# Kernel tuning notes

Hardware: AMD Instinct MI355X
Metric: run time of the kernel (lower is better)

## Reference

```python
import jax, jax.numpy as jnp
import numpy as np

B, C, L = 4, 512, 2048
H, D = 8, C // 8  # n_heads, attention_size


def conv1d_same(x, w, b):
    # x: [B, C, L], w: [Cout, Cin, 3], b: [Cout]; padding='same'
    y = jax.lax.conv_general_dilated(x, w, window_strides=(1,), padding='SAME',
                                     dimension_numbers=('NCH', 'OIH', 'NCH'))
    return y + b[None, :, None]


def setup_inputs() -> dict:
    key = jax.random.key(0)
    ks = jax.random.split(key, 11)
    s = 0.02
    inp = {
        'q': jax.random.normal(ks[0], (B, C, L), jnp.float32),
        'k': jax.random.normal(ks[1], (B, C, L), jnp.float32),
        'v': jax.random.normal(ks[2], (B, C, L), jnp.float32),
        'wq_w': jax.random.normal(ks[3], (C, C, 3), jnp.float32) * s,
        'wq_b': jnp.zeros((C,), jnp.float32),
        'wk_w': jax.random.normal(ks[4], (C, C, 3), jnp.float32) * s,
        'wk_b': jnp.zeros((C,), jnp.float32),
        'wv_w': jax.random.normal(ks[5], (C, C, 3), jnp.float32) * s,
        'wv_b': jnp.zeros((C,), jnp.float32),
        'fc_w': jax.random.normal(ks[6], (C, C, 3), jnp.float32) * s,
        'fc_b': jnp.zeros((C,), jnp.float32),
    }
    return inp


def reference(q, k, v, wq_w, wq_b, wk_w, wk_b, wv_w, wv_b, fc_w, fc_b):
    b = q.shape[0]
    # Faithful to torch: conv output [B,C,L] is row-major reshaped to [B,L,H,D]
    qh = conv1d_same(q, wq_w, wq_b).reshape(b, -1, H, D).transpose(0, 2, 1, 3)  # [B,H,L,D]
    kh = conv1d_same(k, wk_w, wk_b).reshape(b, -1, H, D).transpose(0, 2, 3, 1)  # [B,H,D,L]
    vh = conv1d_same(v, wv_w, wv_b).reshape(b, -1, H, D).transpose(0, 2, 1, 3)  # [B,H,L,D]
    # NOTE: original divides by attention_size D, not sqrt(D)
    attn = jax.nn.softmax(jnp.matmul(qh, kh) / D, axis=-1)  # [B,H,L,L]
    out = jnp.matmul(attn, vh)                               # [B,H,L,D]
    out = out.transpose(0, 2, 1, 3).reshape(b, H * D, -1)    # [B,C,L]
    return conv1d_same(out, fc_w, fc_b)
```

## Files before the change

### kernel.cpp

```cpp
#include <hip/hip_runtime.h>
#include <hip/hip_bf16.h>

#define BB 4
#define NH 8
#define HD 64
#define CC 512
#define LL 2048
#define KK 1536
#define LPAD 2050

typedef float f32x4 __attribute__((ext_vector_type(4)));
typedef short bf16x8 __attribute__((ext_vector_type(8)));

static __device__ __forceinline__ ushort f2bf(float f) {
  union { float f; unsigned u; } v; v.f = f;
  unsigned r = v.u + 0x7fffu + ((v.u >> 16) & 1u);
  return (ushort)(r >> 16);
}
static __device__ __forceinline__ void gload16(const ushort* g, ushort* l) {
  __builtin_amdgcn_global_load_lds((const __attribute__((address_space(1))) void*)g,
                                   (__attribute__((address_space(3))) void*)l, 16, 0, 0);
}

__global__ void prep_w(const float* __restrict__ w0, const float* __restrict__ w1,
                       const float* __restrict__ w2, const float* __restrict__ w3,
                       ushort* __restrict__ out)
{
  int i = blockIdx.x * 256 + threadIdx.x;
  const int per = CC * KK;
  if (i >= 4 * per) return;
  int cidx = i / per;
  int rem  = i - cidx * per;
  int co   = rem / KK;
  int kk   = rem - co * KK;
  int t = kk >> 9, ci = kk & 511;
  const float* w = (cidx == 0) ? w0 : (cidx == 1) ? w1 : (cidx == 2) ? w2 : w3;
  out[i] = f2bf(w[((size_t)co * CC + ci) * 3 + t]);
}

__device__ __forceinline__ void transpose_body(const float* __restrict__ xb,
                                               ushort* __restrict__ ob)
{
  const int c0 = blockIdx.y * 64;
  const int l0 = blockIdx.x * 64;
  const int tid = threadIdx.x;
  __shared__ ushort T[64 * 72];
  {
    const int rr = tid >> 4;
    const int f4 = tid & 15;
#pragma unroll
    for (int it = 0; it < 4; ++it) {
      const int cc = rr + it * 16;
      ushort s[4];
      float4 vv = *(const float4*)(xb + (size_t)(c0 + cc) * LL + l0 + f4 * 4);
      s[0] = f2bf(vv.x); s[1] = f2bf(vv.y); s[2] = f2bf(vv.z); s[3] = f2bf(vv.w);
      *(ushort4*)&T[cc * 72 + f4 * 4] = *(ushort4*)s;
    }
  }
  __syncthreads();
  {
    const int lr = tid >> 3;
    const int ch = tid & 7;
#pragma unroll
    for (int it = 0; it < 2; ++it) {
      const int ll = lr + it * 32;
      ushort tmp[8];
#pragma unroll
      for (int e = 0; e < 8; ++e) tmp[e] = T[(ch * 8 + e) * 72 + ll];
      *(uint4*)(ob + (size_t)(l0 + ll + 1) * CC + c0 + ch * 8) = *(uint4*)tmp;
    }
  }
  if (blockIdx.x == 0 && tid < 8) {
    uint4 z4 = make_uint4(0, 0, 0, 0);
    *(uint4*)(ob + c0 + tid * 8) = z4;
  }
  if (blockIdx.x == (LL / 64 - 1) && tid >= 248) {
    uint4 z4 = make_uint4(0, 0, 0, 0);
    *(uint4*)(ob + (size_t)(LPAD - 1) * CC + c0 + (tid - 248) * 8) = z4;
  }
}

__global__ __launch_bounds__(256, 4)
void transpose_k(const float* __restrict__ in, ushort* __restrict__ outT)
{
  const int b = blockIdx.z;
  transpose_body(in + (size_t)b * CC * LL, outT + (size_t)b * (LPAD * CC));
}

__global__ __launch_bounds__(256, 4)
void transpose3_k(const float* __restrict__ q, const float* __restrict__ k,
                  const float* __restrict__ v, ushort* __restrict__ xq,
                  ushort* __restrict__ xk, ushort* __restrict__ xv)
{
  const int z = blockIdx.z;
  const int b = z & 3, var = z >> 2;
  const float* in = (var == 0) ? q : (var == 1) ? k : v;
  ushort* out = (var == 0) ? xq : (var == 1) ? xk : xv;
  transpose_body(in + (size_t)b * CC * LL, out + (size_t)b * (LPAD * CC));
}

template<int BM>
__device__ __forceinline__ void conv_body(const ushort* __restrict__ xb,
                                          const ushort* __restrict__ Wt,
                                          const float* __restrict__ bias,
                                          void* __restrict__ outp, int mode, int b)
{
  const int co0 = blockIdx.y * BM;
  const int l0  = blockIdx.x * 128;
  const int tid = threadIdx.x;
  const int lane = tid & 63;
  const int w    = tid >> 6;
  const int col  = lane & 15, quad = lane >> 4;
  constexpr int MI = BM / 32;

  __shared__ ushort Asl[BM * 64];
  __shared__ ushort Bsl[128 * 64];

  const int sr = tid >> 3;
  const int g8 = ((tid & 7) ^ (sr & 7)) * 8;
  const ushort* ag  = Wt + (size_t)(co0 + sr) * KK + g8;
  const ushort* bg  = xb + (size_t)(l0 + sr) * CC + g8;
  ushort* alds = &Asl[tid * 8];
  ushort* blds = &Bsl[tid * 8];

  f32x4 acc[MI][4] = {};
  const int wm = (w & 1) * (BM / 2);
  const int wn = (w >> 1) * 64;
  const int c7 = col & 7;

  for (int k0 = 0; k0 < KK; k0 += 64) {
#pragma unroll
    for (int r2 = 0; r2 < MI; ++r2)
      gload16(ag + (size_t)(r2 * 32) * KK + k0, alds + r2 * 2048);
#pragma unroll
    for (int r2 = 0; r2 < 4; ++r2)
      gload16(bg + (size_t)(r2 * 32) * CC + k0, blds + r2 * 2048);
    __syncthreads();
#pragma unroll
    for (int kk = 0; kk < 2; ++kk) {
      bf16x8 af[MI], bfr[4];
#pragma unroll
      for (int i = 0; i < MI; ++i)
        af[i] = *(const bf16x8*)&Asl[(wm + i * 16 + col) * 64 + (((kk * 4 + quad) ^ c7) * 8)];
#pragma unroll
      for (int j = 0; j < 4; ++j)
        bfr[j] = *(const bf16x8*)&Bsl[(wn + j * 16 + col) * 64 + (((kk * 4 + quad) ^ c7) * 8)];
#pragma unroll
      for (int i = 0; i < MI; ++i)
#pragma unroll
        for (int j = 0; j < 4; ++j)
          acc[i][j] = __builtin_amdgcn_mfma_f32_16x16x32_bf16(af[i], bfr[j], acc[i][j], 0, 0, 0);
    }
    __syncthreads();
  }

#pragma unroll
  for (int i = 0; i < MI; ++i) {
#pragma unroll
    for (int r = 0; r < 4; ++r) {
      const int co = co0 + wm + i * 16 + quad * 4 + r;
      const float bi = bias[co];
#pragma unroll
      for (int j = 0; j < 4; ++j) {
        const int l = l0 + wn + j * 16 + col;
        const float y = acc[i][j][r] + bi;
        if (mode == 0) {
          const int xx = (co << 2) + (l >> 9);
          const int hh = (l >> 6) & 7;
          const int dd = l & 63;
          ((ushort*)outp)[((size_t)(b * NH + hh) * LL + xx) * HD + dd] = f2bf(y);
        } else if (mode == 1) {
          const int xx = (co << 2) + (l >> 9);
          const int hh = (l >> 6) & 7;
          const int dd = l & 63;
          ((ushort*)outp)[((size_t)(b * NH + hh) * HD + dd) * LL + xx] = f2bf(y);
        } else {
          ((float*)outp)[(size_t)(b * CC + co) * LL + l] = y;
        }
      }
    }
  }
}

template<int BM>
__global__ __launch_bounds__(256, 3)
void conv_k(const ushort* __restrict__ xT, const ushort* __restrict__ Wt,
            const float* __restrict__ bias, void* __restrict__ outp, int mode)
{
  const int b = blockIdx.z;
  conv_body<BM>(xT + (size_t)b * (LPAD * CC), Wt, bias, outp, mode, b);
}

__global__ __launch_bounds__(256, 3)
void conv3_k(const ushort* __restrict__ xq, const ushort* __restrict__ xk,
             const ushort* __restrict__ xv, const ushort* __restrict__ Wt,
             const float* __restrict__ b0, const float* __restrict__ b1,
             const float* __restrict__ b2, ushort* __restrict__ o0,
             ushort* __restrict__ o1, ushort* __restrict__ o2)
{
  const int z = blockIdx.z;
  const int b = z & 3, var = z >> 2;
  const ushort* xT = (var == 0) ? xq : (var == 1) ? xk : xv;
  const float* bias = (var == 0) ? b0 : (var == 1) ? b1 : b2;
  ushort* outp = (var == 0) ? o0 : (var == 1) ? o1 : o2;
  conv_body<128>(xT + (size_t)b * (LPAD * CC), Wt + (size_t)var * CC * KK, bias, outp,
                 (var == 2) ? 1 : 0, b);
}

__global__ __launch_bounds__(256, 2)
void attn_k(const ushort* __restrict__ qh, const ushort* __restrict__ kh,
            const ushort* __restrict__ vt, ushort* __restrict__ obT)
{
  const int id   = blockIdx.x;
  const int xcd  = id & 7;
  const int slot = id >> 3;
  const int bh   = xcd * 4 + (slot >> 4);
  const int x0   = (slot & 15) * 128;
  const int b = bh >> 3, h = bh & 7;
  const int tid = threadIdx.x, lane = tid & 63, wv = tid >> 6;
  const int col = lane & 15, quad = lane >> 4;
  const int wx = wv * 32;
  const int c7 = col & 7;

  __shared__ ushort Kv[2][8192];
  __shared__ ushort Ps[128 * 88];

  const ushort* Qg = qh + (size_t)bh * (LL * HD);
  const ushort* Kg = kh + (size_t)bh * (LL * HD);
  const ushort* Vg = vt + (size_t)bh * (HD * LL);
  ushort* ob = obT + (size_t)b * (LPAD * CC);

  const int sr = tid >> 3;
  const int g8 = ((tid & 7) ^ (sr & 7)) * 8;

  bf16x8 aq[2][2];
#pragma unroll
  for (int i = 0; i < 2; ++i)
#pragma unroll
    for (int kk = 0; kk < 2; ++kk)
      aq[i][kk] = *(const bf16x8*)(Qg + (size_t)(x0 + wx + i * 16 + col) * HD + kk * 32 + quad * 8);

  const short one = (short)0x3F80;
  const bf16x8 ones = {one, one, one, one, one, one, one, one};

  f32x4 oacc[2][4] = {};
  f32x4 dacc[2] = {};

  {
    ushort* kb = &Kv[0][tid * 8];
    gload16(Kg + (size_t)sr * HD + g8, kb);
    gload16(Kg + (size_t)(32 + sr) * HD + g8, kb + 2048);
    gload16(Vg + (size_t)sr * LL + g8, kb + 4096);
    gload16(Vg + (size_t)(32 + sr) * LL + g8, kb + 6144);
  }

  for (int yt = 0; yt < 32; ++yt) {
    const int cur = yt & 1;
    __syncthreads();
    if (yt + 1 < 32) {
      const int y1 = (yt + 1) * 64;
      ushort* kb = &Kv[1 - cur][tid * 8];
      gload16(Kg + (size_t)(y1 + sr) * HD + g8, kb);
      gload16(Kg + (size_t)(y1 + 32 + sr) * HD + g8, kb + 2048);
      gload16(Vg + (size_t)sr * LL + y1 + g8, kb + 4096);
      gload16(Vg + (size_t)(32 + sr) * LL + y1 + g8, kb + 6144);
    }
    const ushort* Kb = &Kv[cur][0];
    const ushort* Vb = &Kv[cur][4096];

    f32x4 sacc[4][2] = {};
#pragma unroll
    for (int kk = 0; kk < 2; ++kk)
#pragma unroll
      for (int j = 0; j < 4; ++j) {
        bf16x8 bk = *(const bf16x8*)&Kb[(j * 16 + col) * 64 + (((kk * 4 + quad) ^ c7) * 8)];
        sacc[j][0] = __builtin_amdgcn_mfma_f32_16x16x32_bf16(bk, aq[0][kk], sacc[j][0], 0, 0, 0);
        sacc[j][1] = __builtin_amdgcn_mfma_f32_16x16x32_bf16(bk, aq[1][kk], sacc[j][1], 0, 0, 0);
      }
#pragma unroll
    for (int j = 0; j < 4; ++j)
#pragma unroll
      for (int i = 0; i < 2; ++i) {
        union { __hip_bfloat162 h[2]; uint2 u; } pk;
        pk.h[0] = __float22bfloat162_rn(make_float2(__expf(sacc[j][i][0] * 0.015625f),
                                                   __expf(sacc[j][i][1] * 0.015625f)));
        pk.h[1] = __float22bfloat162_rn(make_float2(__expf(sacc[j][i][2] * 0.015625f),
                                                   __expf(sacc[j][i][3] * 0.015625f)));
        *(uint2*)&Ps[(wx + i * 16 + col) * 88 + j * 16 + quad * 4] = pk.u;
      }
#pragma unroll
    for (int kk = 0; kk < 2; ++kk) {
      bf16x8 ap0 = *(const bf16x8*)&Ps[(wx + col) * 88 + kk * 32 + quad * 8];
      bf16x8 ap1 = *(const bf16x8*)&Ps[(wx + 16 + col) * 88 + kk * 32 + quad * 8];
      dacc[0] = __builtin_amdgcn_mfma_f32_16x16x32_bf16(ap0, ones, dacc[0], 0, 0, 0);
      dacc[1] = __builtin_amdgcn_mfma_f32_16x16x32_bf16(ap1, ones, dacc[1], 0, 0, 0);
#pragma unroll
      for (int j = 0; j < 4; ++j) {
        bf16x8 bv = *(const bf16x8*)&Vb[(j * 16 + col) * 64 + (((kk * 4 + quad) ^ c7) * 8)];
        oacc[0][j] = __builtin_amdgcn_mfma_f32_16x16x32_bf16(ap0, bv, oacc[0][j], 0, 0, 0);
        oacc[1][j] = __builtin_amdgcn_mfma_f32_16x16x32_bf16(ap1, bv, oacc[1][j], 0, 0, 0);
      }
    }
  }

#pragma unroll
  for (int i = 0; i < 2; ++i) {
#pragma unroll
    for (int r = 0; r < 4; ++r) {
      const int xg = x0 + wx + i * 16 + quad * 4 + r;
      const float inv = 1.f / dacc[i][r];
#pragma unroll
      for (int j = 0; j < 4; ++j) {
        const int d = j * 16 + col;
        const int flat = xg * 512 + h * 64 + d;
        const int c = flat >> 11, l = flat & 2047;
        ob[(size_t)(l + 1) * CC + c] = f2bf(oacc[i][j][r] * inv);
      }
    }
  }
  if ((slot & 15) == 0 && tid < 128) {
    const int rw = tid >> 6;
    const int cc = h * 64 + (tid & 63);
    ob[(size_t)(rw ? (LPAD - 1) : 0) * CC + cc] = 0;
  }
}

extern "C" void kernel_launch(void* const* d_in, const int* in_sizes, int n_in,
                              void* d_out, int out_size, void* d_ws, size_t ws_size,
                              hipStream_t stream) {
  const float* q    = (const float*)d_in[0];
  const float* k    = (const float*)d_in[1];
  const float* v    = (const float*)d_in[2];
  const float* wq_w = (const float*)d_in[3];
  const float* wq_b = (const float*)d_in[4];
  const float* wk_w = (const float*)d_in[5];
  const float* wk_b = (const float*)d_in[6];
  const float* wv_w = (const float*)d_in[7];
  const float* wv_b = (const float*)d_in[8];
  const float* fc_w = (const float*)d_in[9];
  const float* fc_b = (const float*)d_in[10];

  char* ws = (char*)d_ws;
  const size_t WSZ = (size_t)CC * KK * sizeof(ushort);
  const size_t HSZ = (size_t)BB * NH * LL * HD * sizeof(ushort);
  const size_t XSZ = (size_t)BB * LPAD * CC * sizeof(ushort);
  const size_t FUSED_NEED = 4 * WSZ + 3 * HSZ + 3 * XSZ;

  ushort* Wt = (ushort*)(ws);
  prep_w<<<(4 * CC * KK + 255) / 256, 256, 0, stream>>>(wq_w, wk_w, wv_w, fc_w, Wt);

  if (ws_size >= FUSED_NEED) {
    ushort* qh  = (ushort*)(ws + 4 * WSZ);
    ushort* kh  = (ushort*)(ws + 4 * WSZ + HSZ);
    ushort* vt  = (ushort*)(ws + 4 * WSZ + 2 * HSZ);
    ushort* xTq = (ushort*)(ws + 4 * WSZ + 3 * HSZ);
    ushort* xTk = (ushort*)(ws + 4 * WSZ + 3 * HSZ + XSZ);
    ushort* xTv = (ushort*)(ws + 4 * WSZ + 3 * HSZ + 2 * XSZ);
    ushort* obT = xTq;

    transpose3_k<<<dim3(32, 8, 12), 256, 0, stream>>>(q, k, v, xTq, xTk, xTv);
    conv3_k<<<dim3(16, 4, 12), 256, 0, stream>>>(xTq, xTk, xTv, Wt,
                                                 wq_b, wk_b, wv_b, qh, kh, vt);
    attn_k<<<512, 256, 0, stream>>>(qh, kh, vt, obT);
    conv_k<64><<<dim3(16, 8, 4), 256, 0, stream>>>(obT, Wt + 3 * CC * KK, fc_b,
                                                   (float*)d_out, 2);
  } else {
    ushort* qh  = (ushort*)(ws + 4 * WSZ);
    ushort* kh  = (ushort*)(ws + 4 * WSZ + HSZ);
    ushort* vt  = (ushort*)(ws + 4 * WSZ + 2 * HSZ);
    ushort* xTb = (ushort*)(ws + 4 * WSZ + 3 * HSZ);
    ushort* obT = xTb;

    transpose_k<<<dim3(32, 8, 4), 256, 0, stream>>>(q, xTb);
    conv_k<128><<<dim3(16, 4, 4), 256, 0, stream>>>(xTb, Wt + 0 * CC * KK, wq_b, qh, 0);
    transpose_k<<<dim3(32, 8, 4), 256, 0, stream>>>(k, xTb);
    conv_k<128><<<dim3(16, 4, 4), 256, 0, stream>>>(xTb, Wt + 1 * CC * KK, wk_b, kh, 0);
    transpose_k<<<dim3(32, 8, 4), 256, 0, stream>>>(v, xTb);
    conv_k<128><<<dim3(16, 4, 4), 256, 0, stream>>>(xTb, Wt + 2 * CC * KK, wv_b, vt, 1);
    attn_k<<<512, 256, 0, stream>>>(qh, kh, vt, obT);
    conv_k<64><<<dim3(16, 8, 4), 256, 0, stream>>>(obT, Wt + 3 * CC * KK, fc_b,
                                                   (float*)d_out, 2);
  }
}
```

Baseline: 257.3 us.

## Fold softmax scale into Q conv epilogue and double attention block threads

The Q projection epilogue now multiplies by log2(e)/D, so the attention kernel can use raw exp2 instead of a scaled expf. The attention kernel moves to 512 threads per block with each wave owning 16 query rows instead of 32. The per-wave accumulators and Q fragments shrink, which is meant to raise occupancy and give more waves to hide latency. Each thread now issues half as many K/V tile loads. In exchange there are more waves per block to synchronize, and each wave reuses each K/V fragment for fewer MFMAs, raising LDS read traffic per MFMA.

```diff
diff --git a/kernel.cpp b/kernel.cpp
--- a/kernel.cpp
+++ b/kernel.cpp
@@ -8,6 +8,8 @@
 #define LL 2048
 #define KK 1536
 #define LPAD 2050
+
+#define QS 0.022542110013890054f
 
 typedef float f32x4 __attribute__((ext_vector_type(4)));
 typedef short bf16x8 __attribute__((ext_vector_type(8)));
@@ -103,7 +105,8 @@
 __device__ __forceinline__ void conv_body(const ushort* __restrict__ xb,
                                           const ushort* __restrict__ Wt,
                                           const float* __restrict__ bias,
-                                          void* __restrict__ outp, int mode, int b)
+                                          void* __restrict__ outp, int mode, int b,
+                                          float scale)
 {
   const int co0 = blockIdx.y * BM;
   const int l0  = blockIdx.x * 128;
@@ -163,7 +166,7 @@
 #pragma unroll
       for (int j = 0; j < 4; ++j) {
         const int l = l0 + wn + j * 16 + col;
-        const float y = acc[i][j][r] + bi;
+        const float y = (acc[i][j][r] + bi) * scale;
         if (mode == 0) {
           const int xx = (co << 2) + (l >> 9);
           const int hh = (l >> 6) & 7;
@@ -185,10 +188,11 @@
 template<int BM>
 __global__ __launch_bounds__(256, 3)
 void conv_k(const ushort* __restrict__ xT, const ushort* __restrict__ Wt,
-            const float* __restrict__ bias, void* __restrict__ outp, int mode)
+            const float* __restrict__ bias, void* __restrict__ outp, int mode,
+            float scale)
 {
   const int b = blockIdx.z;
-  conv_body<BM>(xT + (size_t)b * (LPAD * CC), Wt, bias, outp, mode, b);
+  conv_body<BM>(xT + (size_t)b * (LPAD * CC), Wt, bias, outp, mode, b, scale);
 }
 
 __global__ __launch_bounds__(256, 3)
@@ -203,11 +207,12 @@
   const ushort* xT = (var == 0) ? xq : (var == 1) ? xk : xv;
   const float* bias = (var == 0) ? b0 : (var == 1) ? b1 : b2;
   ushort* outp = (var == 0) ? o0 : (var == 1) ? o1 : o2;
+  const float scale = (var == 0) ? QS : 1.0f;
   conv_body<128>(xT + (size_t)b * (LPAD * CC), Wt + (size_t)var * CC * KK, bias, outp,
-                 (var == 2) ? 1 : 0, b);
-}
-
-__global__ __launch_bounds__(256, 2)
+                 (var == 2) ? 1 : 0, b, scale);
+}
+
+__global__ __launch_bounds__(512, 4)
 void attn_k(const ushort* __restrict__ qh, const ushort* __restrict__ kh,
             const ushort* __restrict__ vt, ushort* __restrict__ obT)
 {
@@ -219,7 +224,7 @@
   const int b = bh >> 3, h = bh & 7;
   const int tid = threadIdx.x, lane = tid & 63, wv = tid >> 6;
   const int col = lane & 15, quad = lane >> 4;
-  const int wx = wv * 32;
+  const int wx = wv * 16;
   const int c7 = col & 7;
 
   __shared__ ushort Kv[2][8192];
@@ -233,25 +238,20 @@
   const int sr = tid >> 3;
   const int g8 = ((tid & 7) ^ (sr & 7)) * 8;
 
-  bf16x8 aq[2][2];
-#pragma unroll
-  for (int i = 0; i < 2; ++i)
-#pragma unroll
-    for (int kk = 0; kk < 2; ++kk)
-      aq[i][kk] = *(const bf16x8*)(Qg + (size_t)(x0 + wx + i * 16 + col) * HD + kk * 32 + quad * 8);
+  bf16x8 aq[2];
+#pragma unroll
+  for (int kk = 0; kk < 2; ++kk)
+    aq[kk] = *(const bf16x8*)(Qg + (size_t)(x0 + wx + col) * HD + kk * 32 + quad * 8);
 
   const short one = (short)0x3F80;
   const bf16x8 ones = {one, one, one, one, one, one, one, one};
 
-  f32x4 oacc[2][4] = {};
-  f32x4 dacc[2] = {};
+  f32x4 oacc[4] = {};
+  f32x4 dacc = {};
 
   {
-    ushort* kb = &Kv[0][tid * 8];
-    gload16(Kg + (size_t)sr * HD + g8, kb);
-    gload16(Kg + (size_t)(32 + sr) * HD + g8, kb + 2048);
-    gload16(Vg + (size_t)sr * LL + g8, kb + 4096);
-    gload16(Vg + (size_t)(32 + sr) * LL + g8, kb + 6144);
+    gload16(Kg + (size_t)sr * HD + g8, &Kv[0][tid * 8]);
+    gload16(Vg + (size_t)sr * LL + g8, &Kv[0][4096 + tid * 8]);
   }
 
   for (int yt = 0; yt < 32; ++yt) {
@@ -259,63 +259,51 @@
     __syncthreads();
     if (yt + 1 < 32) {
       const int y1 = (yt + 1) * 64;
-      ushort* kb = &Kv[1 - cur][tid * 8];
-      gload16(Kg + (size_t)(y1 + sr) * HD + g8, kb);
-      gload16(Kg + (size_t)(y1 + 32 + sr) * HD + g8, kb + 2048);
-      gload16(Vg + (size_t)sr * LL + y1 + g8, kb + 4096);
-      gload16(Vg + (size_t)(32 + sr) * LL + y1 + g8, kb + 6144);
+      gload16(Kg + (size_t)(y1 + sr) * HD + g8, &Kv[1 - cur][tid * 8]);
+      gload16(Vg + (size_t)sr * LL + y1 + g8, &Kv[1 - cur][4096 + tid * 8]);
     }
     const ushort* Kb = &Kv[cur][0];
     const ushort* Vb = &Kv[cur][4096];
 
-    f32x4 sacc[4][2] = {};
+    f32x4 sacc[4] = {};
 #pragma unroll
     for (int kk = 0; kk < 2; ++kk)
 #pragma unroll
       for (int j = 0; j < 4; ++j) {
         bf16x8 bk = *(const bf16x8*)&Kb[(j * 16 + col) * 64 + (((kk * 4 + quad) ^ c7) * 8)];
-        sacc[j][0] = __builtin_amdgcn_mfma_f32_16x16x32_bf16(bk, aq[0][kk], sacc[j][0], 0, 0, 0);
-        sacc[j][1] = __builtin_amdgcn_mfma_f32_16x16x32_bf16(bk, aq[1][kk], sacc[j][1], 0, 0, 0);
+        sacc[j] = __builtin_amdgcn_mfma_f32_16x16x32_bf16(bk, aq[kk], sacc[j], 0, 0, 0);
       }
 #pragma unroll
-    for (int j = 0; j < 4; ++j)
-#pragma unroll
-      for (int i = 0; i < 2; ++i) {
-        union { __hip_bfloat162 h[2]; uint2 u; } pk;
-        pk.h[0] = __float22bfloat162_rn(make_float2(__expf(sacc[j][i][0] * 0.015625f),
-                                                   __expf(sacc[j][i][1] * 0.015625f)));
-        pk.h[1] = __float22bfloat162_rn(make_float2(__expf(sacc[j][i][2] * 0.015625f),
-                                                   __expf(sacc[j][i][3] * 0.015625f)));
-        *(uint2*)&Ps[(wx + i * 16 + col) * 88 + j * 16 + quad * 4] = pk.u;
-      }
+    for (int j = 0; j < 4; ++j) {
+      union { __hip_bfloat162 h[2]; uint2 u; } pk;
+      pk.h[0] = __float22bfloat162_rn(make_float2(__builtin_amdgcn_exp2f(sacc[j][0]),
+                                                 __builtin_amdgcn_exp2f(sacc[j][1])));
+      pk.h[1] = __float22bfloat162_rn(make_float2(__builtin_amdgcn_exp2f(sacc[j][2]),
+                                                 __builtin_amdgcn_exp2f(sacc[j][3])));
+      *(uint2*)&Ps[(wx + col) * 88 + j * 16 + quad * 4] = pk.u;
+    }
 #pragma unroll
     for (int kk = 0; kk < 2; ++kk) {
-      bf16x8 ap0 = *(const bf16x8*)&Ps[(wx + col) * 88 + kk * 32 + quad * 8];
-      bf16x8 ap1 = *(const bf16x8*)&Ps[(wx + 16 + col) * 88 + kk * 32 + quad * 8];
-      dacc[0] = __builtin_amdgcn_mfma_f32_16x16x32_bf16(ap0, ones, dacc[0], 0, 0, 0);
-      dacc[1] = __builtin_amdgcn_mfma_f32_16x16x32_bf16(ap1, ones, dacc[1], 0, 0, 0);
+      bf16x8 ap = *(const bf16x8*)&Ps[(wx + col) * 88 + kk * 32 + quad * 8];
+      dacc = __builtin_amdgcn_mfma_f32_16x16x32_bf16(ap, ones, dacc, 0, 0, 0);
 #pragma unroll
       for (int j = 0; j < 4; ++j) {
         bf16x8 bv = *(const bf16x8*)&Vb[(j * 16 + col) * 64 + (((kk * 4 + quad) ^ c7) * 8)];
-        oacc[0][j] = __builtin_amdgcn_mfma_f32_16x16x32_bf16(ap0, bv, oacc[0][j], 0, 0, 0);
-        oacc[1][j] = __builtin_amdgcn_mfma_f32_16x16x32_bf16(ap1, bv, oacc[1][j], 0, 0, 0);
+        oacc[j] = __builtin_amdgcn_mfma_f32_16x16x32_bf16(ap, bv, oacc[j], 0, 0, 0);
       }
     }
   }
 
 #pragma unroll
-  for (int i = 0; i < 2; ++i) {
-#pragma unroll
-    for (int r = 0; r < 4; ++r) {
-      const int xg = x0 + wx + i * 16 + quad * 4 + r;
-      const float inv = 1.f / dacc[i][r];
-#pragma unroll
-      for (int j = 0; j < 4; ++j) {
-        const int d = j * 16 + col;
-        const int flat = xg * 512 + h * 64 + d;
-        const int c = flat >> 11, l = flat & 2047;
-        ob[(size_t)(l + 1) * CC + c] = f2bf(oacc[i][j][r] * inv);
-      }
+  for (int r = 0; r < 4; ++r) {
+    const int xg = x0 + wx + quad * 4 + r;
+    const float inv = 1.f / dacc[r];
+#pragma unroll
+    for (int j = 0; j < 4; ++j) {
+      const int d = j * 16 + col;
+      const int flat = xg * 512 + h * 64 + d;
+      const int c = flat >> 11, l = flat & 2047;
+      ob[(size_t)(l + 1) * CC + c] = f2bf(oacc[j][r] * inv);
     }
   }
   if ((slot & 15) == 0 && tid < 128) {
@@ -361,9 +349,9 @@
     transpose3_k<<<dim3(32, 8, 12), 256, 0, stream>>>(q, k, v, xTq, xTk, xTv);
     conv3_k<<<dim3(16, 4, 12), 256, 0, stream>>>(xTq, xTk, xTv, Wt,
                                                  wq_b, wk_b, wv_b, qh, kh, vt);
-    attn_k<<<512, 256, 0, stream>>>(qh, kh, vt, obT);
+    attn_k<<<512, 512, 0, stream>>>(qh, kh, vt, obT);
     conv_k<64><<<dim3(16, 8, 4), 256, 0, stream>>>(obT, Wt + 3 * CC * KK, fc_b,
-                                                   (float*)d_out, 2);
+                                                   (float*)d_out, 2, 1.0f);
   } else {
     ushort* qh  = (ushort*)(ws + 4 * WSZ);
     ushort* kh  = (ushort*)(ws + 4 * WSZ + HSZ);
@@ -372,13 +360,13 @@
     ushort* obT = xTb;
 
     transpose_k<<<dim3(32, 8, 4), 256, 0, stream>>>(q, xTb);
-    conv_k<128><<<dim3(16, 4, 4), 256, 0, stream>>>(xTb, Wt + 0 * CC * KK, wq_b, qh, 0);
+    conv_k<128><<<dim3(16, 4, 4), 256, 0, stream>>>(xTb, Wt + 0 * CC * KK, wq_b, qh, 0, QS);
     transpose_k<<<dim3(32, 8, 4), 256, 0, stream>>>(k, xTb);
-    conv_k<128><<<dim3(16, 4, 4), 256, 0, stream>>>(xTb, Wt + 1 * CC * KK, wk_b, kh, 0);
+    conv_k<128><<<dim3(16, 4, 4), 256, 0, stream>>>(xTb, Wt + 1 * CC * KK, wk_b, kh, 0, 1.0f);
     transpose_k<<<dim3(32, 8, 4), 256, 0, stream>>>(v, xTb);
-    conv_k<128><<<dim3(16, 4, 4), 256, 0, stream>>>(xTb, Wt + 2 * CC * KK, wv_b, vt, 1);
-    attn_k<<<512, 256, 0, stream>>>(qh, kh, vt, obT);
+    conv_k<128><<<dim3(16, 4, 4), 256, 0, stream>>>(xTb, Wt + 2 * CC * KK, wv_b, vt, 1, 1.0f);
+    attn_k<<<512, 512, 0, stream>>>(qh, kh, vt, obT);
     conv_k<64><<<dim3(16, 8, 4), 256, 0, stream>>>(obT, Wt + 3 * CC * KK, fc_b,
-                                                   (float*)d_out, 2);
-  }
-}
+                                                   (float*)d_out, 2, 1.0f);
+  }
+}
```

Result: no change. 256.8 us (-0.2%).
